# Kernel optimization log

Measured on AMD Instinct MI355X. Metric: run time of the kernel, lower is better.

Reference implementation:

```python
import jax, jax.numpy as jnp
import numpy as np
import math

B, S, HID = 128, 200, 1024
NH = 4
DK = HID // NH
LSESS = 200  # session_len
MAXSEQ = 200
EPS = 1e-12


def setup_inputs() -> dict:
    key = jax.random.key(0)
    ks = jax.random.split(key, 12)
    inp = {}
    inp['query'] = jax.random.normal(ks[0], (B, S, HID), jnp.float32)
    inp['key'] = jax.random.normal(ks[1], (B, S, HID), jnp.float32)
    inp['value'] = jax.random.normal(ks[2], (B, S, HID), jnp.float32)
    std = 0.05
    inp['attn_w0'] = std * jax.random.normal(ks[3], (DK, DK), jnp.float32)
    inp['attn_w1'] = std * jax.random.normal(ks[4], (DK, DK), jnp.float32)
    inp['attn_w2'] = std * jax.random.normal(ks[5], (DK, DK), jnp.float32)
    inp['attn_w3'] = std * jax.random.normal(ks[6], (LSESS, DK), jnp.float32)
    inp['attn_bias'] = jnp.zeros((DK,), jnp.float32)
    inp['complex_weight'] = 0.02 * jax.random.normal(ks[7], (1, NH, MAXSEQ // 2 + 1, DK, 2), jnp.float32)
    bound = 1.0 / math.sqrt(HID)
    inp['linear_w'] = jax.random.uniform(ks[8], (HID, HID), jnp.float32, -bound, bound)
    inp['linear_b'] = jax.random.uniform(ks[9], (HID,), jnp.float32, -bound, bound)
    inp['ln_w'] = jnp.ones((HID,), jnp.float32)
    inp['ln_b'] = jnp.zeros((HID,), jnp.float32)
    return inp


def _gelu(x):
    return x * 0.5 * (1.0 + jax.lax.erf(x / jnp.sqrt(jnp.asarray(2.0, x.dtype))))


def reference(query, key, value, attn_w0, attn_w1, attn_w2, attn_w3, attn_bias,
              complex_weight, linear_w, linear_b, ln_w, ln_b):
    nb = query.shape[0]
    # (B, S, H, DK) -> (B, H, S, DK)
    def split_heads(x):
        return x.reshape(nb, -1, NH, DK).transpose(0, 2, 1, 3)
    q, k, v = split_heads(query), split_heads(key), split_heads(value)

    q = q @ attn_w0
    k = k @ attn_w1
    v = v @ attn_w2

    qf = jnp.fft.rfft(q, axis=2, norm='ortho')   # (B,H,S//2+1,DK) complex
    kf = jnp.fft.rfft(k, axis=2, norm='ortho')
    weight = complex_weight[..., 0] + 1j * complex_weight[..., 1]  # (1,4,MAXSEQ//2+1,DK)
    res = qf * jnp.conj(kf) * weight
    corr = jnp.fft.irfft(res, n=MAXSEQ, axis=2, norm='ortho')       # (B,H,MAXSEQ,DK)

    alpha = jnp.matmul(jax.nn.relu(corr + attn_bias), attn_w3.T)    # (B,H,MAXSEQ,LSESS)
    alpha = jax.nn.softmax(alpha, axis=-2)                          # softmax over seq dim
    x = jnp.einsum('bhsl,bhsd->bhld', alpha, v)                     # (B,H,LSESS,DK)

    x = x.transpose(0, 2, 1, 3).reshape(nb, -1, NH * DK)            # (B,LSESS,HID)
    x = x @ linear_w.T + linear_b
    # dropout is identity at inference
    x = _gelu(x)
    # LayerNorm (TF-style, eps inside sqrt)
    u = x.mean(-1, keepdims=True)
    s = ((x - u) ** 2).mean(-1, keepdims=True)
    x = (x - u) / jnp.sqrt(s + EPS)
    return ln_w * x + ln_b
```

## Files before the change

### kernel.cpp

```cpp
#include <hip/hip_runtime.h>
#include <hip/hip_bf16.h>
#include <math.h>

#define BATCH 128
#define SEQ   200
#define HID   1024
#define NH    4
#define DK    256
#define NF    101
#define LS    200
#define PD    256
#define IMOFF 128

typedef __attribute__((ext_vector_type(8))) short bf16x8;
typedef __attribute__((ext_vector_type(4))) float f32x4;

__device__ __forceinline__ unsigned short f2bf(float f) {
    union { float f; unsigned u; } v; v.f = f;
    unsigned r = v.u + 0x7fff + ((v.u >> 16) & 1);
    return (unsigned short)(r >> 16);
}
__device__ __forceinline__ float bf2f(unsigned short h) {
    union { unsigned u; float f; } v; v.u = ((unsigned)h) << 16;
    return v.f;
}

__device__ __forceinline__ void gld_lds16(const void* g, void* l) {
    __builtin_amdgcn_global_load_lds(
        (const __attribute__((address_space(1))) unsigned*)g,
        (__attribute__((address_space(3))) unsigned*)l, 16, 0, 0);
}

#define KSWZ(row, c8) ((c8) ^ (((row) & 7) << 3))

__global__ void init_tables_bf16(unsigned short* __restrict__ F, unsigned short* __restrict__ G) {
    int idx = blockIdx.x * 256 + threadIdx.x;
    const double inv = 0.07071067811865475244;
    const double PI2 = 6.283185307179586476925;
    {
        int fidx = idx >> 8, s = idx & 255;
        double v = 0.0;
        if (s < SEQ) {
            if (fidx < NF) {
                v = cos(PI2 * (double)((fidx * s) % SEQ) / (double)SEQ) * inv;
            } else if (fidx >= IMOFF && fidx < IMOFF + NF) {
                int f = fidx - IMOFF;
                v = -sin(PI2 * (double)((f * s) % SEQ) / (double)SEQ) * inv;
            }
        }
        F[idx] = f2bf((float)v);
    }
    {
        int s = idx >> 8, j = idx & 255;
        double v = 0.0;
        if (s < SEQ) {
            if (j < NF) {
                double al = (j == 0 || j == NF - 1) ? 1.0 : 2.0;
                v = al * cos(PI2 * (double)((j * s) % SEQ) / (double)SEQ) * inv;
            } else if (j >= IMOFF && j < IMOFF + NF) {
                int f = j - IMOFF;
                if (f != 0 && f != NF - 1)
                    v = -2.0 * sin(PI2 * (double)((f * s) % SEQ) / (double)SEQ) * inv;
            }
        }
        G[idx] = f2bf((float)v);
    }
}

__global__ void wtrans256(const float* __restrict__ src, unsigned short* __restrict__ dst) {
    int dout = blockIdx.x, din = threadIdx.x;
    dst[dout * 256 + din] = f2bf(src[din * 256 + dout]);
}

__global__ void w3pad(const float* __restrict__ src, unsigned short* __restrict__ dst) {
    int row = blockIdx.x, col = threadIdx.x;
    dst[row * 256 + col] = (row < LS) ? f2bf(src[row * 256 + col]) : (unsigned short)0;
}

__global__ void fconv(const float* __restrict__ src, unsigned short* __restrict__ dst, int n) {
    int i = blockIdx.x * 256 + threadIdx.x;
    if (i < n) dst[i] = f2bf(src[i]);
}

__global__ __launch_bounds__(512, 2)
void mgemm256f(const unsigned short* __restrict__ Wall,
               const float* __restrict__ Q, const float* __restrict__ Kt,
               const float* __restrict__ V, unsigned short* __restrict__ C0) {
    __shared__ unsigned short As[256 * 64];
    __shared__ unsigned short Bs[256 * 64];

    int bz = blockIdx.x;
    int sel = bz >> 9;
    int bh = bz & 511;
    int b = bh >> 2, h = bh & 3;
    const unsigned short* A = Wall + sel * 65536;
    const float* Bf = ((sel == 0) ? Q : (sel == 1) ? Kt : V) + (long)b * SEQ * HID + h * DK;
    unsigned short* Ch = C0 + (long)sel * 33554432 + (long)bh * PD * PD;

    int t = threadIdx.x;
    int lane = t & 63, wave = t >> 6;
    int wr = wave >> 2, wc = wave & 3;
    int la = lane & 15, hi = lane >> 4;
    int rsub = t >> 3;
    int c8 = (t & 7) * 8;

    f32x4 acc[8][4] = {};

    for (int k0 = 0; k0 < 256; k0 += 64) {
#pragma unroll
        for (int p = 0; p < 4; ++p) {
            int row = p * 64 + rsub;
            gld_lds16(A + (long)row * 256 + k0 + KSWZ(row, c8), &As[row * 64 + c8]);
        }
#pragma unroll
        for (int p = 0; p < 4; ++p) {
            int row = p * 64 + rsub;
            unsigned short tmp[8];
            if (row < SEQ) {
                const float4* s4 = reinterpret_cast<const float4*>(Bf + (long)row * HID + k0 + c8);
                float4 x0 = s4[0], x1 = s4[1];
                tmp[0] = f2bf(x0.x); tmp[1] = f2bf(x0.y); tmp[2] = f2bf(x0.z); tmp[3] = f2bf(x0.w);
                tmp[4] = f2bf(x1.x); tmp[5] = f2bf(x1.y); tmp[6] = f2bf(x1.z); tmp[7] = f2bf(x1.w);
            } else {
#pragma unroll
                for (int j = 0; j < 8; ++j) tmp[j] = 0;
            }
            *(bf16x8*)&Bs[row * 64 + KSWZ(row, c8)] = *(bf16x8*)tmp;
        }
        __syncthreads();
#pragma unroll
        for (int half = 0; half < 2; ++half) {
            int ko = half * 32 + hi * 8;
            bf16x8 bb[4], xx[8];
#pragma unroll
            for (int ni = 0; ni < 4; ++ni) {
                int rb = wc * 64 + ni * 16 + la;
                bb[ni] = *(const bf16x8*)&Bs[rb * 64 + KSWZ(rb, ko)];
            }
#pragma unroll
            for (int mi = 0; mi < 8; ++mi) {
                int ra = wr * 128 + mi * 16 + la;
                xx[mi] = *(const bf16x8*)&As[ra * 64 + KSWZ(ra, ko)];
            }
            __builtin_amdgcn_s_setprio(1);
#pragma unroll
            for (int mi = 0; mi < 8; ++mi)
#pragma unroll
                for (int ni = 0; ni < 4; ++ni)
                    acc[mi][ni] = __builtin_amdgcn_mfma_f32_16x16x32_bf16(xx[mi], bb[ni], acc[mi][ni], 0, 0, 0);
            __builtin_amdgcn_s_setprio(0);
        }
        __syncthreads();
    }

#pragma unroll
    for (int mi = 0; mi < 8; ++mi) {
#pragma unroll
        for (int ni = 0; ni < 4; ++ni) {
            int gn = wc * 64 + ni * 16 + la;
            int gmB = wr * 128 + mi * 16 + hi * 4;
#pragma unroll
            for (int rr = 0; rr < 4; ++rr)
                Ch[(long)(gmB + rr) * PD + gn] = f2bf(acc[mi][ni][rr]);
        }
    }
}

template <int EPI, bool XCDSWZ>
__global__ __launch_bounds__(512, 2)
void mgemm256(const unsigned short* __restrict__ A, const unsigned short* __restrict__ B,
              unsigned short* __restrict__ C0, int K, int lda, int ldb, int ldc,
              long aOuter, long aInner, long bOuter, long bInner,
              long cOuter, long cInner, int nInner, int mValid,
              const float* __restrict__ biasN) {
    extern __shared__ unsigned short lds[];
    unsigned short* AsB = lds;
    unsigned short* BsB = lds + 32768;

    int bx = blockIdx.x, by = blockIdx.y;
    if (XCDSWZ) {
        int nwg = gridDim.x * gridDim.y;
        int flat = by * gridDim.x + bx;
        int cpx = nwg >> 3;
        int swz = (flat & 7) * cpx + (flat >> 3);
        bx = swz % gridDim.x; by = swz / gridDim.x;
    }
    int bz = blockIdx.z;
    int bo = bz / nInner, bi = bz - bo * nInner;
    const unsigned short* Ab = A + bo * aOuter + bi * aInner;
    const unsigned short* Bb = B + bo * bOuter + bi * bInner;

    int t = threadIdx.x;
    int m0 = by * 256, n0 = bx * 256;
    int lane = t & 63, wave = t >> 6;
    int wr = wave >> 2, wc = wave & 3;
    int la = lane & 15, hi = lane >> 4;

    f32x4 acc[8][4] = {};
    int rsub = t >> 3;
    int c8 = (t & 7) * 8;

    auto stageA = [&](unsigned short* dst, long k0, int h) {
#pragma unroll
        for (int p = 0; p < 2; ++p) {
            int row = h * 128 + p * 64 + rsub;
            gld_lds16(Ab + (long)(m0 + row) * lda + k0 + KSWZ(row, c8), &dst[row * 64 + c8]);
        }
    };
    auto stageB = [&](unsigned short* dst, long k0, int h) {
#pragma unroll
        for (int p = 0; p < 2; ++p) {
            int row = h * 128 + p * 64 + rsub;
            gld_lds16(Bb + (long)(n0 + row) * ldb + k0 + KSWZ(row, c8), &dst[row * 64 + c8]);
        }
    };
    auto ldf = [&](const unsigned short* P, int row, int ko) -> bf16x8 {
        return *(const bf16x8*)&P[row * 64 + KSWZ(row, ko)];
    };

#define MFMA_ROW(mi, xa) \
    acc[mi][0] = __builtin_amdgcn_mfma_f32_16x16x32_bf16(xa, b0, acc[mi][0], 0, 0, 0); \
    acc[mi][1] = __builtin_amdgcn_mfma_f32_16x16x32_bf16(xa, b1, acc[mi][1], 0, 0, 0); \
    acc[mi][2] = __builtin_amdgcn_mfma_f32_16x16x32_bf16(xa, b2, acc[mi][2], 0, 0, 0); \
    acc[mi][3] = __builtin_amdgcn_mfma_f32_16x16x32_bf16(xa, b3, acc[mi][3], 0, 0, 0);

    int nkt = K >> 6;
    stageA(AsB, 0, 0); stageA(AsB, 0, 1);
    stageB(BsB, 0, 0); stageB(BsB, 0, 1);

    for (int kt = 0; kt < nkt; ++kt) {
        int cur = kt & 1;
        const unsigned short* Ac = AsB + cur * 16384;
        const unsigned short* Bc = BsB + cur * 16384;
        unsigned short* An = AsB + (cur ^ 1) * 16384;
        unsigned short* Bn = BsB + (cur ^ 1) * 16384;
        bool pre = (kt + 1) < nkt;
        long kn = (long)(kt + 1) << 6;

        bf16x8 b0, b1, b2, b3;

        if (pre) {
            stageA(An, kn, 0);
            asm volatile("s_waitcnt vmcnt(2)" ::: "memory");
        } else {
            asm volatile("s_waitcnt vmcnt(0)" ::: "memory");
        }
        __builtin_amdgcn_s_barrier();
        __builtin_amdgcn_sched_barrier(0);
        {
            int ko = hi * 8;
            b0 = ldf(Bc, wc * 64 + 0 * 16 + la, ko);
            b1 = ldf(Bc, wc * 64 + 1 * 16 + la, ko);
            b2 = ldf(Bc, wc * 64 + 2 * 16 + la, ko);
            b3 = ldf(Bc, wc * 64 + 3 * 16 + la, ko);
            bf16x8 x0 = ldf(Ac, wr * 128 + 0 * 16 + la, ko);
            bf16x8 x1 = ldf(Ac, wr * 128 + 1 * 16 + la, ko);
            bf16x8 x2 = ldf(Ac, wr * 128 + 2 * 16 + la, ko);
            bf16x8 x3 = ldf(Ac, wr * 128 + 3 * 16 + la, ko);
            __builtin_amdgcn_s_setprio(1);
            MFMA_ROW(0, x0) MFMA_ROW(1, x1) MFMA_ROW(2, x2) MFMA_ROW(3, x3)
            __builtin_amdgcn_s_setprio(0);
        }
        __builtin_amdgcn_s_barrier();

        if (pre) stageA(An, kn, 1);
        {
            int ko = hi * 8;
            bf16x8 x4 = ldf(Ac, wr * 128 + 4 * 16 + la, ko);
            bf16x8 x5 = ldf(Ac, wr * 128 + 5 * 16 + la, ko);
            bf16x8 x6 = ldf(Ac, wr * 128 + 6 * 16 + la, ko);
            bf16x8 x7 = ldf(Ac, wr * 128 + 7 * 16 + la, ko);
            __builtin_amdgcn_s_setprio(1);
            MFMA_ROW(4, x4) MFMA_ROW(5, x5) MFMA_ROW(6, x6) MFMA_ROW(7, x7)
            __builtin_amdgcn_s_setprio(0);
        }
        __builtin_amdgcn_s_barrier();

        if (pre) stageB(Bn, kn, 0);
        {
            int ko = 32 + hi * 8;
            b0 = ldf(Bc, wc * 64 + 0 * 16 + la, ko);
            b1 = ldf(Bc, wc * 64 + 1 * 16 + la, ko);
            b2 = ldf(Bc, wc * 64 + 2 * 16 + la, ko);
            b3 = ldf(Bc, wc * 64 + 3 * 16 + la, ko);
            bf16x8 x0 = ldf(Ac, wr * 128 + 0 * 16 + la, ko);
            bf16x8 x1 = ldf(Ac, wr * 128 + 1 * 16 + la, ko);
            bf16x8 x2 = ldf(Ac, wr * 128 + 2 * 16 + la, ko);
            bf16x8 x3 = ldf(Ac, wr * 128 + 3 * 16 + la, ko);
            __builtin_amdgcn_s_setprio(1);
            MFMA_ROW(0, x0) MFMA_ROW(1, x1) MFMA_ROW(2, x2) MFMA_ROW(3, x3)
            __builtin_amdgcn_s_setprio(0);
        }
        __builtin_amdgcn_s_barrier();

        if (pre) stageB(Bn, kn, 1);
        {
            int ko = 32 + hi * 8;
            bf16x8 x4 = ldf(Ac, wr * 128 + 4 * 16 + la, ko);
            bf16x8 x5 = ldf(Ac, wr * 128 + 5 * 16 + la, ko);
            bf16x8 x6 = ldf(Ac, wr * 128 + 6 * 16 + la, ko);
            bf16x8 x7 = ldf(Ac, wr * 128 + 7 * 16 + la, ko);
            __builtin_amdgcn_s_setprio(1);
            MFMA_ROW(4, x4) MFMA_ROW(5, x5) MFMA_ROW(6, x6) MFMA_ROW(7, x7)
            __builtin_amdgcn_s_setprio(0);
        }
        __builtin_amdgcn_s_barrier();
    }
#undef MFMA_ROW

    unsigned short* Ch = C0 + bo * cOuter + bi * cInner;
#pragma unroll
    for (int mi = 0; mi < 8; ++mi) {
#pragma unroll
        for (int ni = 0; ni < 4; ++ni) {
            int gn = n0 + wc * 64 + ni * 16 + la;
            int gmB = m0 + wr * 128 + mi * 16 + hi * 4;
            float bN = 0.f;
            if (EPI == 2 || EPI == 4) bN = biasN[gn];
#pragma unroll
            for (int rr = 0; rr < 4; ++rr) {
                int gm = gmB + rr;
                if (gm >= mValid) continue;
                float v = acc[mi][ni][rr];
                if (EPI == 0) Ch[(long)gm * ldc + gn] = f2bf(v);
                else if (EPI == 2) Ch[(long)gm * ldc + gn] = f2bf(fmaxf(v + bN, 0.f));
                else Ch[(long)gm * ldc + gn] = f2bf(v + bN);
            }
        }
    }
}

__global__ __launch_bounds__(512, 2)
void alphasm(const unsigned short* __restrict__ A, const unsigned short* __restrict__ B,
             unsigned short* __restrict__ P0) {
    extern __shared__ unsigned short lds[];
    unsigned short* AsB = lds;
    unsigned short* BsB = lds + 32768;
    __shared__ float redM[256][4];
    __shared__ float redS[256][4];

    int bh = blockIdx.x;
    const unsigned short* Ab = A;
    const unsigned short* Bb = B + (long)bh * PD * PD;

    int t = threadIdx.x;
    int lane = t & 63, wave = t >> 6;
    int wr = wave >> 2, wc = wave & 3;
    int la = lane & 15, hi = lane >> 4;

    f32x4 acc[8][4] = {};
    int rsub = t >> 3;
    int c8 = (t & 7) * 8;

    auto stageA = [&](unsigned short* dst, long k0, int h) {
#pragma unroll
        for (int p = 0; p < 2; ++p) {
            int row = h * 128 + p * 64 + rsub;
            gld_lds16(Ab + (long)row * PD + k0 + KSWZ(row, c8), &dst[row * 64 + c8]);
        }
    };
    auto stageB = [&](unsigned short* dst, long k0, int h) {
#pragma unroll
        for (int p = 0; p < 2; ++p) {
            int row = h * 128 + p * 64 + rsub;
            gld_lds16(Bb + (long)row * PD + k0 + KSWZ(row, c8), &dst[row * 64 + c8]);
        }
    };
    auto ldf = [&](const unsigned short* P, int row, int ko) -> bf16x8 {
        return *(const bf16x8*)&P[row * 64 + KSWZ(row, ko)];
    };

#define MFMA_ROW(mi, xa) \
    acc[mi][0] = __builtin_amdgcn_mfma_f32_16x16x32_bf16(xa, b0, acc[mi][0], 0, 0, 0); \
    acc[mi][1] = __builtin_amdgcn_mfma_f32_16x16x32_bf16(xa, b1, acc[mi][1], 0, 0, 0); \
    acc[mi][2] = __builtin_amdgcn_mfma_f32_16x16x32_bf16(xa, b2, acc[mi][2], 0, 0, 0); \
    acc[mi][3] = __builtin_amdgcn_mfma_f32_16x16x32_bf16(xa, b3, acc[mi][3], 0, 0, 0);

    stageA(AsB, 0, 0); stageA(AsB, 0, 1);
    stageB(BsB, 0, 0); stageB(BsB, 0, 1);

    for (int kt = 0; kt < 4; ++kt) {
        int cur = kt & 1;
        const unsigned short* Ac = AsB + cur * 16384;
        const unsigned short* Bc = BsB + cur * 16384;
        unsigned short* An = AsB + (cur ^ 1) * 16384;
        unsigned short* Bn = BsB + (cur ^ 1) * 16384;
        bool pre = kt < 3;
        long kn = (long)(kt + 1) << 6;
        bf16x8 b0, b1, b2, b3;

        if (pre) {
            stageA(An, kn, 0);
            asm volatile("s_waitcnt vmcnt(2)" ::: "memory");
        } else {
            asm volatile("s_waitcnt vmcnt(0)" ::: "memory");
        }
        __builtin_amdgcn_s_barrier();
        __builtin_amdgcn_sched_barrier(0);
        {
            int ko = hi * 8;
            b0 = ldf(Bc, wc * 64 + 0 * 16 + la, ko);
            b1 = ldf(Bc, wc * 64 + 1 * 16 + la, ko);
            b2 = ldf(Bc, wc * 64 + 2 * 16 + la, ko);
            b3 = ldf(Bc, wc * 64 + 3 * 16 + la, ko);
            bf16x8 x0 = ldf(Ac, wr * 128 + 0 * 16 + la, ko);
            bf16x8 x1 = ldf(Ac, wr * 128 + 1 * 16 + la, ko);
            bf16x8 x2 = ldf(Ac, wr * 128 + 2 * 16 + la, ko);
            bf16x8 x3 = ldf(Ac, wr * 128 + 3 * 16 + la, ko);
            __builtin_amdgcn_s_setprio(1);
            MFMA_ROW(0, x0) MFMA_ROW(1, x1) MFMA_ROW(2, x2) MFMA_ROW(3, x3)
            __builtin_amdgcn_s_setprio(0);
        }
        __builtin_amdgcn_s_barrier();
        if (pre) stageA(An, kn, 1);
        {
            int ko = hi * 8;
            bf16x8 x4 = ldf(Ac, wr * 128 + 4 * 16 + la, ko);
            bf16x8 x5 = ldf(Ac, wr * 128 + 5 * 16 + la, ko);
            bf16x8 x6 = ldf(Ac, wr * 128 + 6 * 16 + la, ko);
            bf16x8 x7 = ldf(Ac, wr * 128 + 7 * 16 + la, ko);
            __builtin_amdgcn_s_setprio(1);
            MFMA_ROW(4, x4) MFMA_ROW(5, x5) MFMA_ROW(6, x6) MFMA_ROW(7, x7)
            __builtin_amdgcn_s_setprio(0);
        }
        __builtin_amdgcn_s_barrier();
        if (pre) stageB(Bn, kn, 0);
        {
            int ko = 32 + hi * 8;
            b0 = ldf(Bc, wc * 64 + 0 * 16 + la, ko);
            b1 = ldf(Bc, wc * 64 + 1 * 16 + la, ko);
            b2 = ldf(Bc, wc * 64 + 2 * 16 + la, ko);
            b3 = ldf(Bc, wc * 64 + 3 * 16 + la, ko);
            bf16x8 x0 = ldf(Ac, wr * 128 + 0 * 16 + la, ko);
            bf16x8 x1 = ldf(Ac, wr * 128 + 1 * 16 + la, ko);
            bf16x8 x2 = ldf(Ac, wr * 128 + 2 * 16 + la, ko);
            bf16x8 x3 = ldf(Ac, wr * 128 + 3 * 16 + la, ko);
            __builtin_amdgcn_s_setprio(1);
            MFMA_ROW(0, x0) MFMA_ROW(1, x1) MFMA_ROW(2, x2) MFMA_ROW(3, x3)
            __builtin_amdgcn_s_setprio(0);
        }
        __builtin_amdgcn_s_barrier();
        if (pre) stageB(Bn, kn, 1);
        {
            int ko = 32 + hi * 8;
            bf16x8 x4 = ldf(Ac, wr * 128 + 4 * 16 + la, ko);
            bf16x8 x5 = ldf(Ac, wr * 128 + 5 * 16 + la, ko);
            bf16x8 x6 = ldf(Ac, wr * 128 + 6 * 16 + la, ko);
            bf16x8 x7 = ldf(Ac, wr * 128 + 7 * 16 + la, ko);
            __builtin_amdgcn_s_setprio(1);
            MFMA_ROW(4, x4) MFMA_ROW(5, x5) MFMA_ROW(6, x6) MFMA_ROW(7, x7)
            __builtin_amdgcn_s_setprio(0);
        }
        __builtin_amdgcn_s_barrier();
    }
#undef MFMA_ROW

#pragma unroll
    for (int mi = 0; mi < 8; ++mi) {
#pragma unroll
        for (int rr = 0; rr < 4; ++rr) {
            float mv = -1e30f;
#pragma unroll
            for (int ni = 0; ni < 4; ++ni) {
                int gn = wc * 64 + ni * 16 + la;
                if (gn < LS) mv = fmaxf(mv, acc[mi][ni][rr]);
            }
            mv = fmaxf(mv, __shfl_xor(mv, 1));
            mv = fmaxf(mv, __shfl_xor(mv, 2));
            mv = fmaxf(mv, __shfl_xor(mv, 4));
            mv = fmaxf(mv, __shfl_xor(mv, 8));
            if (la == 0) redM[wr * 128 + mi * 16 + hi * 4 + rr][wc] = mv;
        }
    }
    __syncthreads();
#pragma unroll
    for (int mi = 0; mi < 8; ++mi) {
#pragma unroll
        for (int rr = 0; rr < 4; ++rr) {
            int row = wr * 128 + mi * 16 + hi * 4 + rr;
            float m = fmaxf(fmaxf(redM[row][0], redM[row][1]),
                            fmaxf(redM[row][2], redM[row][3]));
            float s = 0.f;
#pragma unroll
            for (int ni = 0; ni < 4; ++ni) {
                int gn = wc * 64 + ni * 16 + la;
                float e = (gn < LS) ? __expf(acc[mi][ni][rr] - m) : 0.f;
                acc[mi][ni][rr] = e;
                s += e;
            }
            s += __shfl_xor(s, 1);
            s += __shfl_xor(s, 2);
            s += __shfl_xor(s, 4);
            s += __shfl_xor(s, 8);
            if (la == 0) redS[row][wc] = s;
        }
    }
    __syncthreads();
    unsigned short* P = lds;
#pragma unroll
    for (int mi = 0; mi < 8; ++mi) {
#pragma unroll
        for (int rr = 0; rr < 4; ++rr) {
            int row = wr * 128 + mi * 16 + hi * 4 + rr;
            float inv = 1.f / (redS[row][0] + redS[row][1] + redS[row][2] + redS[row][3]);
#pragma unroll
            for (int ni = 0; ni < 4; ++ni) {
                int gn = wc * 64 + ni * 16 + la;
                P[row * 256 + gn] = f2bf(acc[mi][ni][rr] * inv);
            }
        }
    }
    __syncthreads();
    unsigned short* Pg = P0 + (long)bh * PD * PD;
    for (int i = t; i < 256 * 32; i += 512) {
        int row = i >> 5, seg = (i & 31) * 8;
        *(bf16x8*)(Pg + (long)row * PD + seg) = *(const bf16x8*)&P[row * 256 + seg];
    }
}

__global__ __launch_bounds__(256)
void crossspec(unsigned short* __restrict__ QF, const unsigned short* __restrict__ KF,
               const float* __restrict__ cw) {
    int bh = blockIdx.x;
    int h = bh & (NH - 1);
    long qbase = (long)bh * DK * PD;
    for (int i = threadIdx.x; i < DK * 13; i += 256) {
        int d = i / 13, fg = i - d * 13;
        long rb = qbase + (long)d * PD + fg * 8;
        bf16x8 qre = *(const bf16x8*)(QF + rb);
        bf16x8 qim = *(const bf16x8*)(QF + rb + IMOFF);
        bf16x8 kre = *(const bf16x8*)(KF + rb);
        bf16x8 kim = *(const bf16x8*)(KF + rb + IMOFF);
        bf16x8 orr, oii;
#pragma unroll
        for (int j = 0; j < 8; ++j) {
            int f = fg * 8 + j;
            float qr = bf2f((unsigned short)qre[j]), qi = bf2f((unsigned short)qim[j]);
            float kr = bf2f((unsigned short)kre[j]), ki = bf2f((unsigned short)kim[j]);
            float cr = qr * kr + qi * ki;
            float ci = qi * kr - qr * ki;
            float wr = 0.f, wi = 0.f;
            if (f < NF) {
                long wb = (((long)h * NF + f) * DK + d) * 2;
                wr = cw[wb]; wi = cw[wb + 1];
            }
            orr[j] = (short)f2bf(cr * wr - ci * wi);
            oii[j] = (short)f2bf(cr * wi + ci * wr);
        }
        *(bf16x8*)(QF + rb) = orr;
        *(bf16x8*)(QF + rb + IMOFF) = oii;
    }
}

__global__ __launch_bounds__(256) void gelu_ln_kernel(const unsigned short* __restrict__ y2,
                               const float* __restrict__ lnw, const float* __restrict__ lnb,
                               float* __restrict__ out) {
    long row = blockIdx.x;
    int tid = threadIdx.x;
    const short4* xr = reinterpret_cast<const short4*>(y2 + row * HID);
    short4 h4 = xr[tid];
    float g[4];
    {
        float x0 = bf2f((unsigned short)h4.x), x1 = bf2f((unsigned short)h4.y);
        float x2 = bf2f((unsigned short)h4.z), x3 = bf2f((unsigned short)h4.w);
        g[0] = 0.5f * x0 * (1.f + erff(x0 * 0.70710678118654752f));
        g[1] = 0.5f * x1 * (1.f + erff(x1 * 0.70710678118654752f));
        g[2] = 0.5f * x2 * (1.f + erff(x2 * 0.70710678118654752f));
        g[3] = 0.5f * x3 * (1.f + erff(x3 * 0.70710678118654752f));
    }

    __shared__ float red[4];
    float s = g[0] + g[1] + g[2] + g[3];
#pragma unroll
    for (int o = 32; o > 0; o >>= 1) s += __shfl_down(s, o);
    if ((tid & 63) == 0) red[tid >> 6] = s;
    __syncthreads();
    float mean = (red[0] + red[1] + red[2] + red[3]) * (1.f / (float)HID);

    float v2 = 0.f;
#pragma unroll
    for (int p = 0; p < 4; ++p) { float d = g[p] - mean; v2 += d * d; }
    __syncthreads();
#pragma unroll
    for (int o = 32; o > 0; o >>= 1) v2 += __shfl_down(v2, o);
    if ((tid & 63) == 0) red[tid >> 6] = v2;
    __syncthreads();
    float var = (red[0] + red[1] + red[2] + red[3]) * (1.f / (float)HID);
    float rstd = rsqrtf(var + 1e-12f);

    float4 o4;
    int i0 = tid * 4;
    o4.x = (g[0] - mean) * rstd * lnw[i0 + 0] + lnb[i0 + 0];
    o4.y = (g[1] - mean) * rstd * lnw[i0 + 1] + lnb[i0 + 1];
    o4.z = (g[2] - mean) * rstd * lnw[i0 + 2] + lnb[i0 + 2];
    o4.w = (g[3] - mean) * rstd * lnw[i0 + 3] + lnb[i0 + 3];
    reinterpret_cast<float4*>(out + row * HID)[tid] = o4;
}

extern "C" void kernel_launch(void* const* d_in, const int* in_sizes, int n_in,
                              void* d_out, int out_size, void* d_ws, size_t ws_size,
                              hipStream_t stream) {
    const float* query = (const float*)d_in[0];
    const float* key   = (const float*)d_in[1];
    const float* value = (const float*)d_in[2];
    const float* w0 = (const float*)d_in[3];
    const float* w1 = (const float*)d_in[4];
    const float* w2 = (const float*)d_in[5];
    const float* w3 = (const float*)d_in[6];
    const float* attn_bias = (const float*)d_in[7];
    const float* cw = (const float*)d_in[8];
    const float* lw = (const float*)d_in[9];
    const float* lb = (const float*)d_in[10];
    const float* lnw = (const float*)d_in[11];
    const float* lnb = (const float*)d_in[12];
    float* out = (float*)d_out;

    char* base = (char*)d_ws;
    const long BH = (long)BATCH * NH;
    const long SZR = (long)BH * PD * PD;
    const size_t M64 = 67108864;

    unsigned short* F_stack = (unsigned short*)(base + 0);
    unsigned short* G_stack = (unsigned short*)(base + 131072);
    unsigned short* w0T = (unsigned short*)(base + 262144);
    unsigned short* w3b = (unsigned short*)(base + 655360);
    unsigned short* lwb = (unsigned short*)(base + 786432);
    char* rA = base + 4194304;
    char* rB = rA + M64;
    char* rC = rB + M64;
    char* rD = rC + M64;
    char* rE = rD + M64;

    unsigned short* qpT = (unsigned short*)rA;
    unsigned short* kpT = (unsigned short*)rB;
    unsigned short* vpT = (unsigned short*)rC;
    unsigned short* QF  = (unsigned short*)rD;
    unsigned short* KF  = (unsigned short*)rE;
    unsigned short* corr = (unsigned short*)rA;
    unsigned short* probs = (unsigned short*)rB;
    unsigned short* X  = (unsigned short*)rE;
    unsigned short* y2 = (unsigned short*)rD;

    const size_t LDS256 = 131072;

    init_tables_bf16<<<256, 256, 0, stream>>>(F_stack, G_stack);
    wtrans256<<<256, 256, 0, stream>>>(w0, w0T);
    wtrans256<<<256, 256, 0, stream>>>(w1, w0T + 65536);
    wtrans256<<<256, 256, 0, stream>>>(w2, w0T + 131072);
    w3pad<<<256, 256, 0, stream>>>(w3, w3b);
    fconv<<<(HID * HID + 255) / 256, 256, 0, stream>>>(lw, lwb, HID * HID);

    mgemm256f<<<dim3(3 * 512, 1, 1), 512, 0, stream>>>(w0T, query, key, value, qpT);

    mgemm256<0, false><<<dim3(1, 1, 2 * BH), 512, LDS256, stream>>>(
        qpT, F_stack, QF, PD, PD, PD, PD,
        SZR, (long)PD * PD, 0L, 0L, SZR, (long)PD * PD, (int)BH, PD, nullptr);

    crossspec<<<(unsigned)BH, 256, 0, stream>>>(QF, KF, cw);

    mgemm256<2, false><<<dim3(1, 1, BH), 512, LDS256, stream>>>(
        G_stack, QF, corr, PD, PD, PD, PD,
        0L, 0L, (long)PD * PD, 0L, (long)PD * PD, 0L, 1, PD, attn_bias);

    alphasm<<<dim3((unsigned)BH, 1, 1), 512, LDS256, stream>>>(w3b, corr, probs);

    mgemm256<0, false><<<dim3(1, 1, BH), 512, LDS256, stream>>>(
        probs, vpT, X, PD, PD, PD, HID,
        (long)NH * PD * PD, (long)PD * PD,
        (long)NH * PD * PD, (long)PD * PD,
        (long)LS * HID, (long)DK, NH, LS, nullptr);

    mgemm256<4, true><<<dim3(HID / 256, (BATCH * LS) / 256, 1), 512, LDS256, stream>>>(
        X, lwb, y2, HID, HID, HID, HID,
        0L, 0L, 0L, 0L, 0L, 0L, 1, BATCH * LS, lb);

    gelu_ln_kernel<<<(unsigned)(BATCH * LS), 256, 0, stream>>>(y2, lnw, lnb, out);
}
```

Measured before the change: 613.8 us.

## Double-buffer the fp32-input projection GEMM with register-prefetched loads

The Q/K/V projection GEMM now double-buffers its LDS tiles and issues the next k-tile's global loads (A via direct-to-LDS, B fp32 via inline-asm dwordx4 into registers) before computing the current tile. The aim is to hide global memory latency behind the MFMA work. In exchange it uses 128KB of dynamic LDS with occupancy 1 block per CU instead of 2, and relies on manual waitcnt and barrier placement. Out-of-range rows are clamped to row 0 and then zero-filled.

```diff
diff --git a/kernel.cpp b/kernel.cpp
--- a/kernel.cpp
+++ b/kernel.cpp
@@ -29,6 +29,12 @@
     __builtin_amdgcn_global_load_lds(
         (const __attribute__((address_space(1))) unsigned*)g,
         (__attribute__((address_space(3))) unsigned*)l, 16, 0, 0);
+}
+
+__device__ __forceinline__ float4 gl4(const float* p) {
+    float4 r;
+    asm volatile("global_load_dwordx4 %0, %1, off" : "=v"(r) : "v"(p));
+    return r;
 }
 
 #define KSWZ(row, c8) ((c8) ^ (((row) & 7) << 3))
@@ -82,12 +88,13 @@
     if (i < n) dst[i] = f2bf(src[i]);
 }
 
-__global__ __launch_bounds__(512, 2)
-void mgemm256f(const unsigned short* __restrict__ Wall,
-               const float* __restrict__ Q, const float* __restrict__ Kt,
-               const float* __restrict__ V, unsigned short* __restrict__ C0) {
-    __shared__ unsigned short As[256 * 64];
-    __shared__ unsigned short Bs[256 * 64];
+__global__ __launch_bounds__(512, 1)
+void mgemm256fp(const unsigned short* __restrict__ Wall,
+                const float* __restrict__ Q, const float* __restrict__ Kt,
+                const float* __restrict__ V, unsigned short* __restrict__ C0) {
+    extern __shared__ unsigned short lds[];
+    unsigned short* AsB = lds;
+    unsigned short* BsB = lds + 32768;
 
     int bz = blockIdx.x;
     int sel = bz >> 9;
@@ -105,29 +112,73 @@
     int c8 = (t & 7) * 8;
 
     f32x4 acc[8][4] = {};
-
-    for (int k0 = 0; k0 < 256; k0 += 64) {
+    float4 br0, br1, br2, br3, br4, br5, br6, br7;
+
+    bool val[4];
+    int rowv[4];
+#pragma unroll
+    for (int p = 0; p < 4; ++p) {
+        int row = p * 64 + rsub;
+        val[p] = row < SEQ;
+        rowv[p] = val[p] ? row : 0;
+    }
+
+    auto issueA = [&](unsigned short* dstAs, long k0) {
 #pragma unroll
         for (int p = 0; p < 4; ++p) {
             int row = p * 64 + rsub;
-            gld_lds16(A + (long)row * 256 + k0 + KSWZ(row, c8), &As[row * 64 + c8]);
-        }
+            gld_lds16(A + (long)row * 256 + k0 + KSWZ(row, c8), &dstAs[row * 64 + c8]);
+        }
+    };
+    auto issueB = [&](long k0) {
+        const float* p0 = Bf + (long)rowv[0] * HID + k0 + c8;
+        const float* p1 = Bf + (long)rowv[1] * HID + k0 + c8;
+        const float* p2 = Bf + (long)rowv[2] * HID + k0 + c8;
+        const float* p3 = Bf + (long)rowv[3] * HID + k0 + c8;
+        br0 = gl4(p0); br1 = gl4(p0 + 4);
+        br2 = gl4(p1); br3 = gl4(p1 + 4);
+        br4 = gl4(p2); br5 = gl4(p2 + 4);
+        br6 = gl4(p3); br7 = gl4(p3 + 4);
+    };
+    auto writeB = [&](unsigned short* dstBs) {
+        float4 lo[4] = {br0, br2, br4, br6};
+        float4 hi4[4] = {br1, br3, br5, br7};
 #pragma unroll
         for (int p = 0; p < 4; ++p) {
             int row = p * 64 + rsub;
             unsigned short tmp[8];
-            if (row < SEQ) {
-                const float4* s4 = reinterpret_cast<const float4*>(Bf + (long)row * HID + k0 + c8);
-                float4 x0 = s4[0], x1 = s4[1];
+            if (val[p]) {
+                float4 x0 = lo[p], x1 = hi4[p];
                 tmp[0] = f2bf(x0.x); tmp[1] = f2bf(x0.y); tmp[2] = f2bf(x0.z); tmp[3] = f2bf(x0.w);
                 tmp[4] = f2bf(x1.x); tmp[5] = f2bf(x1.y); tmp[6] = f2bf(x1.z); tmp[7] = f2bf(x1.w);
             } else {
 #pragma unroll
                 for (int j = 0; j < 8; ++j) tmp[j] = 0;
             }
-            *(bf16x8*)&Bs[row * 64 + KSWZ(row, c8)] = *(bf16x8*)tmp;
-        }
-        __syncthreads();
+            *(bf16x8*)&dstBs[row * 64 + KSWZ(row, c8)] = *(bf16x8*)tmp;
+        }
+    };
+
+    issueA(AsB, 0);
+    issueB(0);
+
+    for (int kt = 0; kt < 4; ++kt) {
+        int cur = kt & 1;
+        unsigned short* Ac = AsB + cur * 16384;
+        unsigned short* Bc = BsB + cur * 16384;
+
+        asm volatile("s_waitcnt vmcnt(0)" ::: "memory");
+        __builtin_amdgcn_sched_barrier(0);
+        writeB(Bc);
+        if (kt < 3) {
+            long kn = (long)(kt + 1) << 6;
+            issueA(AsB + (cur ^ 1) * 16384, kn);
+            issueB(kn);
+        }
+        asm volatile("s_waitcnt lgkmcnt(0)" ::: "memory");
+        __builtin_amdgcn_s_barrier();
+        __builtin_amdgcn_sched_barrier(0);
+
 #pragma unroll
         for (int half = 0; half < 2; ++half) {
             int ko = half * 32 + hi * 8;
@@ -135,12 +186,12 @@
 #pragma unroll
             for (int ni = 0; ni < 4; ++ni) {
                 int rb = wc * 64 + ni * 16 + la;
-                bb[ni] = *(const bf16x8*)&Bs[rb * 64 + KSWZ(rb, ko)];
+                bb[ni] = *(const bf16x8*)&Bc[rb * 64 + KSWZ(rb, ko)];
             }
 #pragma unroll
             for (int mi = 0; mi < 8; ++mi) {
                 int ra = wr * 128 + mi * 16 + la;
-                xx[mi] = *(const bf16x8*)&As[ra * 64 + KSWZ(ra, ko)];
+                xx[mi] = *(const bf16x8*)&Ac[ra * 64 + KSWZ(ra, ko)];
             }
             __builtin_amdgcn_s_setprio(1);
 #pragma unroll
@@ -150,7 +201,7 @@
                     acc[mi][ni] = __builtin_amdgcn_mfma_f32_16x16x32_bf16(xx[mi], bb[ni], acc[mi][ni], 0, 0, 0);
             __builtin_amdgcn_s_setprio(0);
         }
-        __syncthreads();
+        __builtin_amdgcn_s_barrier();
     }
 
 #pragma unroll
@@ -650,7 +701,7 @@
     w3pad<<<256, 256, 0, stream>>>(w3, w3b);
     fconv<<<(HID * HID + 255) / 256, 256, 0, stream>>>(lw, lwb, HID * HID);
 
-    mgemm256f<<<dim3(3 * 512, 1, 1), 512, 0, stream>>>(w0T, query, key, value, qpT);
+    mgemm256fp<<<dim3(3 * 512, 1, 1), 512, LDS256, stream>>>(w0T, query, key, value, qpT);
 
     mgemm256<0, false><<<dim3(1, 1, 2 * BH), 512, LDS256, stream>>>(
         qpT, F_stack, QF, PD, PD, PD, PD,
```

Result: slower. 634.8 us (+3.4%).

## Split input projection into bf16 conversion plus pipelined GEMM; widen crossspec grid

Applied to the files above, without the earlier changes.

Replaces the fused fp32-loading projection GEMM with separate vectorized fp32-to-bf16 conversion kernels followed by three launches of the generic pipelined mgemm256. mgemm256 gains an nValid column bound so that rows past the sequence length are not stored. The cross-spectrum kernel is split into 16 blocks per batch-head instead of one, to raise parallelism. The new path adds an extra bf16 round trip through global memory for the inputs and leaves padded output columns unwritten, relying on later stages to ignore them.

```diff
diff --git a/kernel.cpp b/kernel.cpp
--- a/kernel.cpp
+++ b/kernel.cpp
@@ -82,87 +82,17 @@
     if (i < n) dst[i] = f2bf(src[i]);
 }
 
-__global__ __launch_bounds__(512, 2)
-void mgemm256f(const unsigned short* __restrict__ Wall,
-               const float* __restrict__ Q, const float* __restrict__ Kt,
-               const float* __restrict__ V, unsigned short* __restrict__ C0) {
-    __shared__ unsigned short As[256 * 64];
-    __shared__ unsigned short Bs[256 * 64];
-
-    int bz = blockIdx.x;
-    int sel = bz >> 9;
-    int bh = bz & 511;
-    int b = bh >> 2, h = bh & 3;
-    const unsigned short* A = Wall + sel * 65536;
-    const float* Bf = ((sel == 0) ? Q : (sel == 1) ? Kt : V) + (long)b * SEQ * HID + h * DK;
-    unsigned short* Ch = C0 + (long)sel * 33554432 + (long)bh * PD * PD;
-
-    int t = threadIdx.x;
-    int lane = t & 63, wave = t >> 6;
-    int wr = wave >> 2, wc = wave & 3;
-    int la = lane & 15, hi = lane >> 4;
-    int rsub = t >> 3;
-    int c8 = (t & 7) * 8;
-
-    f32x4 acc[8][4] = {};
-
-    for (int k0 = 0; k0 < 256; k0 += 64) {
-#pragma unroll
-        for (int p = 0; p < 4; ++p) {
-            int row = p * 64 + rsub;
-            gld_lds16(A + (long)row * 256 + k0 + KSWZ(row, c8), &As[row * 64 + c8]);
-        }
-#pragma unroll
-        for (int p = 0; p < 4; ++p) {
-            int row = p * 64 + rsub;
-            unsigned short tmp[8];
-            if (row < SEQ) {
-                const float4* s4 = reinterpret_cast<const float4*>(Bf + (long)row * HID + k0 + c8);
-                float4 x0 = s4[0], x1 = s4[1];
-                tmp[0] = f2bf(x0.x); tmp[1] = f2bf(x0.y); tmp[2] = f2bf(x0.z); tmp[3] = f2bf(x0.w);
-                tmp[4] = f2bf(x1.x); tmp[5] = f2bf(x1.y); tmp[6] = f2bf(x1.z); tmp[7] = f2bf(x1.w);
-            } else {
-#pragma unroll
-                for (int j = 0; j < 8; ++j) tmp[j] = 0;
-            }
-            *(bf16x8*)&Bs[row * 64 + KSWZ(row, c8)] = *(bf16x8*)tmp;
-        }
-        __syncthreads();
-#pragma unroll
-        for (int half = 0; half < 2; ++half) {
-            int ko = half * 32 + hi * 8;
-            bf16x8 bb[4], xx[8];
-#pragma unroll
-            for (int ni = 0; ni < 4; ++ni) {
-                int rb = wc * 64 + ni * 16 + la;
-                bb[ni] = *(const bf16x8*)&Bs[rb * 64 + KSWZ(rb, ko)];
-            }
-#pragma unroll
-            for (int mi = 0; mi < 8; ++mi) {
-                int ra = wr * 128 + mi * 16 + la;
-                xx[mi] = *(const bf16x8*)&As[ra * 64 + KSWZ(ra, ko)];
-            }
-            __builtin_amdgcn_s_setprio(1);
-#pragma unroll
-            for (int mi = 0; mi < 8; ++mi)
-#pragma unroll
-                for (int ni = 0; ni < 4; ++ni)
-                    acc[mi][ni] = __builtin_amdgcn_mfma_f32_16x16x32_bf16(xx[mi], bb[ni], acc[mi][ni], 0, 0, 0);
-            __builtin_amdgcn_s_setprio(0);
-        }
-        __syncthreads();
-    }
-
-#pragma unroll
-    for (int mi = 0; mi < 8; ++mi) {
-#pragma unroll
-        for (int ni = 0; ni < 4; ++ni) {
-            int gn = wc * 64 + ni * 16 + la;
-            int gmB = wr * 128 + mi * 16 + hi * 4;
-#pragma unroll
-            for (int rr = 0; rr < 4; ++rr)
-                Ch[(long)(gmB + rr) * PD + gn] = f2bf(acc[mi][ni][rr]);
-        }
+__global__ __launch_bounds__(256)
+void convbf(const float* __restrict__ src, unsigned short* __restrict__ dst, int n8) {
+    int i = blockIdx.x * 256 + threadIdx.x;
+    int stride = gridDim.x * 256;
+    for (; i < n8; i += stride) {
+        const float4* s4 = reinterpret_cast<const float4*>(src + (long)i * 8);
+        float4 x0 = s4[0], x1 = s4[1];
+        unsigned short tmp[8];
+        tmp[0] = f2bf(x0.x); tmp[1] = f2bf(x0.y); tmp[2] = f2bf(x0.z); tmp[3] = f2bf(x0.w);
+        tmp[4] = f2bf(x1.x); tmp[5] = f2bf(x1.y); tmp[6] = f2bf(x1.z); tmp[7] = f2bf(x1.w);
+        *(bf16x8*)(dst + (long)i * 8) = *(bf16x8*)tmp;
     }
 }
 
@@ -171,7 +101,7 @@
 void mgemm256(const unsigned short* __restrict__ A, const unsigned short* __restrict__ B,
               unsigned short* __restrict__ C0, int K, int lda, int ldb, int ldc,
               long aOuter, long aInner, long bOuter, long bInner,
-              long cOuter, long cInner, int nInner, int mValid,
+              long cOuter, long cInner, int nInner, int mValid, int nValid,
               const float* __restrict__ biasN) {
     extern __shared__ unsigned short lds[];
     unsigned short* AsB = lds;
@@ -314,6 +244,7 @@
 #pragma unroll
         for (int ni = 0; ni < 4; ++ni) {
             int gn = n0 + wc * 64 + ni * 16 + la;
+            if (gn >= nValid) continue;
             int gmB = m0 + wr * 128 + mi * 16 + hi * 4;
             float bN = 0.f;
             if (EPI == 2 || EPI == 4) bN = biasN[gn];
@@ -521,35 +452,37 @@
 __global__ __launch_bounds__(256)
 void crossspec(unsigned short* __restrict__ QF, const unsigned short* __restrict__ KF,
                const float* __restrict__ cw) {
-    int bh = blockIdx.x;
+    int blk = blockIdx.x;
+    int bh = blk >> 4;
+    int d0 = (blk & 15) * 16;
     int h = bh & (NH - 1);
-    long qbase = (long)bh * DK * PD;
-    for (int i = threadIdx.x; i < DK * 13; i += 256) {
-        int d = i / 13, fg = i - d * 13;
-        long rb = qbase + (long)d * PD + fg * 8;
-        bf16x8 qre = *(const bf16x8*)(QF + rb);
-        bf16x8 qim = *(const bf16x8*)(QF + rb + IMOFF);
-        bf16x8 kre = *(const bf16x8*)(KF + rb);
-        bf16x8 kim = *(const bf16x8*)(KF + rb + IMOFF);
-        bf16x8 orr, oii;
-#pragma unroll
-        for (int j = 0; j < 8; ++j) {
-            int f = fg * 8 + j;
-            float qr = bf2f((unsigned short)qre[j]), qi = bf2f((unsigned short)qim[j]);
-            float kr = bf2f((unsigned short)kre[j]), ki = bf2f((unsigned short)kim[j]);
-            float cr = qr * kr + qi * ki;
-            float ci = qi * kr - qr * ki;
-            float wr = 0.f, wi = 0.f;
-            if (f < NF) {
-                long wb = (((long)h * NF + f) * DK + d) * 2;
-                wr = cw[wb]; wi = cw[wb + 1];
-            }
-            orr[j] = (short)f2bf(cr * wr - ci * wi);
-            oii[j] = (short)f2bf(cr * wi + ci * wr);
-        }
-        *(bf16x8*)(QF + rb) = orr;
-        *(bf16x8*)(QF + rb + IMOFF) = oii;
-    }
+    int t = threadIdx.x;
+    if (t >= 16 * 13) return;
+    int dl = t / 13, fg = t - dl * 13;
+    int d = d0 + dl;
+    long rb = (long)bh * DK * PD + (long)d * PD + fg * 8;
+    bf16x8 qre = *(const bf16x8*)(QF + rb);
+    bf16x8 qim = *(const bf16x8*)(QF + rb + IMOFF);
+    bf16x8 kre = *(const bf16x8*)(KF + rb);
+    bf16x8 kim = *(const bf16x8*)(KF + rb + IMOFF);
+    bf16x8 orr, oii;
+#pragma unroll
+    for (int j = 0; j < 8; ++j) {
+        int f = fg * 8 + j;
+        float qr = bf2f((unsigned short)qre[j]), qi = bf2f((unsigned short)qim[j]);
+        float kr = bf2f((unsigned short)kre[j]), ki = bf2f((unsigned short)kim[j]);
+        float cr = qr * kr + qi * ki;
+        float ci = qi * kr - qr * ki;
+        float wr = 0.f, wi = 0.f;
+        if (f < NF) {
+            long wb = (((long)h * NF + f) * DK + d) * 2;
+            wr = cw[wb]; wi = cw[wb + 1];
+        }
+        orr[j] = (short)f2bf(cr * wr - ci * wi);
+        oii[j] = (short)f2bf(cr * wi + ci * wr);
+    }
+    *(bf16x8*)(QF + rb) = orr;
+    *(bf16x8*)(QF + rb + IMOFF) = oii;
 }
 
 __global__ __launch_bounds__(256) void gelu_ln_kernel(const unsigned short* __restrict__ y2,
@@ -619,6 +552,7 @@
     const long BH = (long)BATCH * NH;
     const long SZR = (long)BH * PD * PD;
     const size_t M64 = 67108864;
+    const int NQ8 = BATCH * SEQ * HID / 8;
 
     unsigned short* F_stack = (unsigned short*)(base + 0);
     unsigned short* G_stack = (unsigned short*)(base + 131072);
@@ -634,6 +568,8 @@
     unsigned short* qpT = (unsigned short*)rA;
     unsigned short* kpT = (unsigned short*)rB;
     unsigned short* vpT = (unsigned short*)rC;
+    unsigned short* qbD = (unsigned short*)rD;
+    unsigned short* qbE = (unsigned short*)rE;
     unsigned short* QF  = (unsigned short*)rD;
     unsigned short* KF  = (unsigned short*)rE;
     unsigned short* corr = (unsigned short*)rA;
@@ -650,17 +586,31 @@
     w3pad<<<256, 256, 0, stream>>>(w3, w3b);
     fconv<<<(HID * HID + 255) / 256, 256, 0, stream>>>(lw, lwb, HID * HID);
 
-    mgemm256f<<<dim3(3 * 512, 1, 1), 512, 0, stream>>>(w0T, query, key, value, qpT);
+    convbf<<<2048, 256, 0, stream>>>(query, qbD, NQ8);
+    convbf<<<2048, 256, 0, stream>>>(key, qbE, NQ8);
+    mgemm256<0, false><<<dim3(1, 1, BH), 512, LDS256, stream>>>(
+        w0T, qbD, qpT, DK, DK, HID, PD,
+        0L, 0L, (long)SEQ * HID, (long)DK,
+        (long)NH * PD * PD, (long)PD * PD, NH, PD, SEQ, nullptr);
+    mgemm256<0, false><<<dim3(1, 1, BH), 512, LDS256, stream>>>(
+        w0T + 65536, qbE, kpT, DK, DK, HID, PD,
+        0L, 0L, (long)SEQ * HID, (long)DK,
+        (long)NH * PD * PD, (long)PD * PD, NH, PD, SEQ, nullptr);
+    convbf<<<2048, 256, 0, stream>>>(value, qbD, NQ8);
+    mgemm256<0, false><<<dim3(1, 1, BH), 512, LDS256, stream>>>(
+        w0T + 131072, qbD, vpT, DK, DK, HID, PD,
+        0L, 0L, (long)SEQ * HID, (long)DK,
+        (long)NH * PD * PD, (long)PD * PD, NH, PD, SEQ, nullptr);
 
     mgemm256<0, false><<<dim3(1, 1, 2 * BH), 512, LDS256, stream>>>(
         qpT, F_stack, QF, PD, PD, PD, PD,
-        SZR, (long)PD * PD, 0L, 0L, SZR, (long)PD * PD, (int)BH, PD, nullptr);
-
-    crossspec<<<(unsigned)BH, 256, 0, stream>>>(QF, KF, cw);
+        SZR, (long)PD * PD, 0L, 0L, SZR, (long)PD * PD, (int)BH, PD, PD, nullptr);
+
+    crossspec<<<(unsigned)(BH * 16), 256, 0, stream>>>(QF, KF, cw);
 
     mgemm256<2, false><<<dim3(1, 1, BH), 512, LDS256, stream>>>(
         G_stack, QF, corr, PD, PD, PD, PD,
-        0L, 0L, (long)PD * PD, 0L, (long)PD * PD, 0L, 1, PD, attn_bias);
+        0L, 0L, (long)PD * PD, 0L, (long)PD * PD, 0L, 1, PD, PD, attn_bias);
 
     alphasm<<<dim3((unsigned)BH, 1, 1), 512, LDS256, stream>>>(w3b, corr, probs);
 
@@ -668,11 +618,11 @@
         probs, vpT, X, PD, PD, PD, HID,
         (long)NH * PD * PD, (long)PD * PD,
         (long)NH * PD * PD, (long)PD * PD,
-        (long)LS * HID, (long)DK, NH, LS, nullptr);
+        (long)LS * HID, (long)DK, NH, LS, PD, nullptr);
 
     mgemm256<4, true><<<dim3(HID / 256, (BATCH * LS) / 256, 1), 512, LDS256, stream>>>(
         X, lwb, y2, HID, HID, HID, HID,
-        0L, 0L, 0L, 0L, 0L, 0L, 1, BATCH * LS, lb);
+        0L, 0L, 0L, 0L, 0L, 0L, 1, BATCH * LS, HID, lb);
 
     gelu_ln_kernel<<<(unsigned)(BATCH * LS), 256, 0, stream>>>(y2, lnw, lnb, out);
 }
```

Result: slower. 660.5 us (+7.6%).
